# Kernel tuning notes

Measured on AMD Instinct MI355X. Metric: run time of the kernel, lower is better.

The kernel has to match this reference:

```python
import jax, jax.numpy as jnp
import numpy as np

D_MODEL = 1024
NUM_HEADS = 16

def _dense_params(key, d_in, d_out):
    kw, _ = jax.random.split(key)
    # flax default: lecun_normal kernel, zeros bias
    W = jax.random.normal(kw, (d_in, d_out), dtype=jnp.float32) / np.sqrt(d_in)
    b = jnp.zeros((d_out,), dtype=jnp.float32)
    return W, b

def setup_inputs() -> dict:
    key = jax.random.key(0)
    ks = jax.random.split(key, 8)
    B, Tx, Tc = 2, 2048, 2048
    x = jax.random.normal(ks[0], (B, Tx, D_MODEL), dtype=jnp.float32)
    context = jax.random.normal(ks[1], (B, Tc, D_MODEL), dtype=jnp.float32)
    Wq, bq = _dense_params(ks[2], D_MODEL, D_MODEL)
    Wks, bks = _dense_params(ks[3], D_MODEL, D_MODEL)
    Wvs, bvs = _dense_params(ks[4], D_MODEL, D_MODEL)
    Wkc, bkc = _dense_params(ks[5], D_MODEL, D_MODEL)
    Wvc, bvc = _dense_params(ks[6], D_MODEL, D_MODEL)
    Wo, bo = _dense_params(ks[7], D_MODEL, D_MODEL)
    return {"x": x, "context": context,
            "Wq": Wq, "bq": bq, "Wks": Wks, "bks": bks, "Wvs": Wvs, "bvs": bvs,
            "Wkc": Wkc, "bkc": bkc, "Wvc": Wvc, "bvc": bvc, "Wo": Wo, "bo": bo}

def _split_heads(t, H):
    B, T, C = t.shape
    return t.reshape(B, T, H, C // H).transpose(0, 2, 1, 3)  # [B,H,T,hd]

def reference(x, context, Wq, bq, Wks, bks, Wvs, bvs, Wkc, bkc, Wvc, bvc, Wo, bo):
    H = NUM_HEADS
    head_dim = D_MODEL // H
    q = x @ Wq + bq
    k = jnp.concatenate([x @ Wks + bks, context @ Wkc + bkc], axis=1)
    v = jnp.concatenate([x @ Wvs + bvs, context @ Wvc + bvc], axis=1)
    q = _split_heads(q, H)  # [B,H,Tq,hd]
    k = _split_heads(k, H)  # [B,H,Tk,hd]
    v = _split_heads(v, H)
    attn = jnp.einsum('bhqd,bhkd->bhqk', q, k) / jnp.sqrt(jnp.float32(head_dim))
    attn = jax.nn.softmax(attn, axis=-1)
    out = jnp.einsum('bhqk,bhkd->bhqd', attn, v)
    B, _, Tq, _ = out.shape
    out = out.transpose(0, 2, 1, 3).reshape(B, Tq, D_MODEL)
    return out @ Wo + bo
```

## Files before the change

kernel.cpp:

```cpp
#include <hip/hip_runtime.h>
#include <hip/hip_bf16.h>
#include <math.h>


typedef _Float16 f16;
typedef _Float16 f16x8 __attribute__((ext_vector_type(8)));
typedef _Float16 f16x4v __attribute__((ext_vector_type(4)));
typedef float    f32x4 __attribute__((ext_vector_type(4)));

#define MFMA_F16(a, b, c) __builtin_amdgcn_mfma_f32_16x16x32_f16((a), (b), (c), 0, 0, 0)

#define QSCALE 0.18033688011112042f

__device__ __forceinline__ void glds16(const f16* g, f16* l) {
    __builtin_amdgcn_global_load_lds(
        (const __attribute__((address_space(1))) void*)g,
        (__attribute__((address_space(3))) void*)l, 16, 0, 0);
}

__global__ __launch_bounds__(256) void prep(
    const float4* __restrict__ x, const float4* __restrict__ ctx,
    f16x4v* __restrict__ xb, f16x4v* __restrict__ cb,
    const float* __restrict__ W0, const float* __restrict__ W1,
    const float* __restrict__ W2, const float* __restrict__ W3,
    const float* __restrict__ W4, const float* __restrict__ W5,
    f16* __restrict__ wt)
{
    if (blockIdx.x < 8192) {
        const int n4 = (2 * 2048 * 1024) / 4;
        int i = blockIdx.x * 256 + threadIdx.x;
        float4 v;
        f16x4v* dst;
        if (i < n4) { v = x[i];        dst = xb + i; }
        else        { v = ctx[i - n4]; dst = cb + (i - n4); }
        f16x4v h = { (f16)v.x, (f16)v.y, (f16)v.z, (f16)v.w };
        *dst = h;
        return;
    }
    const int idx = blockIdx.x - 8192;
    const int z = idx >> 10, rem = idx & 1023;
    const float* Ws[6] = { W0, W1, W2, W3, W4, W5 };
    const float* W = Ws[z];
    f16* Wt = wt + (size_t)z * (1024 * 1024);

    __shared__ float tile[32][33];
    const int tx = threadIdx.x & 31, ty = threadIdx.x >> 5;
    const int n0 = (rem & 31) * 32, k0 = (rem >> 5) * 32;

#pragma unroll
    for (int i = 0; i < 4; ++i) {
        int r = i * 8 + ty;
        tile[r][tx] = W[(size_t)(k0 + r) * 1024 + n0 + tx];
    }
    __syncthreads();
#pragma unroll
    for (int i = 0; i < 4; ++i) {
        int r = i * 8 + ty;
        Wt[(size_t)(n0 + r) * 1024 + k0 + tx] = (f16)tile[tx][r];
    }
}

#define GEMM_PROLOGUE(BN)                                                     \
    const int m0 = blockIdx.x * 128, n0 = blockIdx.y * (BN);                  \
    const int tid = threadIdx.x;                                              \
    const int w = tid >> 6, lane = tid & 63, quad = lane >> 4, l15 = lane & 15;\
    const int wm = (w >> 1) * 64, wn = (w & 1) * ((BN) / 2);                  \
    const int qsw = (quad ^ ((l15 >> 1) & 3)) * 8;                            \
    int gA[2], gB[(BN) / 64];                                                 \
    _Pragma("unroll")                                                         \
    for (int p = 0; p < 2; ++p) {                                             \
        int s = tid + p * 256;                                                \
        int r = (s >> 2) & 127, c = (s & 3) ^ ((s >> 3) & 3);                 \
        gA[p] = (m0 + r) * 1024 + c * 8;                                      \
    }                                                                         \
    _Pragma("unroll")                                                         \
    for (int p = 0; p < (BN) / 64; ++p) {                                     \
        int s = tid + p * 256;                                                \
        int r = (s >> 2) & ((BN) - 1), c = (s & 3) ^ ((s >> 3) & 3);          \
        gB[p] = (n0 + r) * 1024 + c * 8;                                      \
    }

#define GEMM_STAGE(BN)                                                        \
    __syncthreads();                                                          \
    _Pragma("unroll")                                                         \
    for (int p = 0; p < 2; ++p) glds16(&A[gA[p] + k0], &As[(p * 256 + w * 64) * 8]); \
    _Pragma("unroll")                                                         \
    for (int p = 0; p < (BN) / 64; ++p) glds16(&Bt[gB[p] + k0], &Bs[(p * 256 + w * 64) * 8]); \
    __syncthreads();

__global__ __launch_bounds__(256) void proj_gemm(
    const f16* __restrict__ xb, const f16* __restrict__ cb,
    const f16* __restrict__ wt,
    const float* __restrict__ bq, const float* __restrict__ bks,
    const float* __restrict__ bkc, const float* __restrict__ bvs,
    const float* __restrict__ bvc,
    f16* __restrict__ qbuf, f16* __restrict__ kbuf, f16* __restrict__ vbuf)
{
    __shared__ alignas(16) f16 As[128 * 32];
    __shared__ alignas(16) f16 Bs[128 * 32];

    const int z = blockIdx.z;
    const f16* A = (z == 0 || z == 1 || z == 3) ? xb : cb;
    const int wslot = (z == 0) ? 0 : (z == 1) ? 1 : (z == 2) ? 3 : (z == 3) ? 2 : 4;
    const f16* Bt = wt + (size_t)wslot * 1048576;
    const float* bias = (z == 0) ? bq : (z == 1) ? bks : (z == 2) ? bkc
                        : (z == 3) ? bvs : bvc;
    const int roff = (z == 2 || z == 4) ? 2048 : 0;

    GEMM_PROLOGUE(128)
    f32x4 acc[4][4] = {};

    for (int k0 = 0; k0 < 1024; k0 += 32) {
        GEMM_STAGE(128)
        f16x8 a[4], b[4];
#pragma unroll
        for (int i = 0; i < 4; ++i)
            a[i] = *(const f16x8*)&As[(wm + i * 16 + l15) * 32 + qsw];
#pragma unroll
        for (int i = 0; i < 4; ++i)
            b[i] = *(const f16x8*)&Bs[(wn + i * 16 + l15) * 32 + qsw];
#pragma unroll
        for (int mi = 0; mi < 4; ++mi)
#pragma unroll
            for (int ni = 0; ni < 4; ++ni)
                acc[mi][ni] = MFMA_F16(a[mi], b[ni], acc[mi][ni]);
    }

#pragma unroll
    for (int mi = 0; mi < 4; ++mi) {
#pragma unroll
        for (int r = 0; r < 4; ++r) {
            int row = m0 + wm + mi * 16 + quad * 4 + r;
            int b_ = row >> 11, tok = row & 2047;
#pragma unroll
            for (int ni = 0; ni < 4; ++ni) {
                int col = n0 + wn + ni * 16 + l15;
                float v = acc[mi][ni][r] + bias[col];
                int bh = b_ * 16 + (col >> 6);
                int tg = roff + tok;
                if (z == 0) {
                    qbuf[((size_t)bh * 2048 + tok) * 64 + (col & 63)] = (f16)(v * QSCALE);
                } else if (z <= 2) {
                    kbuf[(size_t)bh * 262144 + (size_t)(tg >> 6) * 4096
                         + (size_t)((col >> 5) & 1) * 2048 + (tg & 63) * 32 + (col & 31)] = (f16)v;
                } else {
                    vbuf[(size_t)bh * 262144 + (size_t)tg * 64 + (col & 63)] = (f16)v;
                }
            }
        }
    }
}

__global__ __launch_bounds__(256) void transpose_v(
    const f16* __restrict__ vbuf, f16* __restrict__ vt)
{
    const int t = threadIdx.x;
    const int mt = t >> 3, md = t & 7;
    const int tok0 = blockIdx.x * 256 + mt * 8;
    const int z = blockIdx.y;
    f16x8 in[8];
#pragma unroll
    for (int i = 0; i < 8; ++i)
        in[i] = *(const f16x8*)&vbuf[((size_t)z * 4096 + tok0 + i) * 64 + md * 8];
    f16x8 ov[8];
#pragma unroll
    for (int j = 0; j < 8; ++j)
#pragma unroll
        for (int i = 0; i < 8; ++i) ov[j][i] = in[i][j];
    const int kt = tok0 >> 6, kks = (tok0 >> 5) & 1, kko = tok0 & 31;
#pragma unroll
    for (int j = 0; j < 8; ++j)
        *(f16x8*)&vt[(size_t)z * 262144 + (size_t)kt * 4096 + kks * 2048
                     + (md * 8 + j) * 32 + kko] = ov[j];
}

__global__ __launch_bounds__(128) void attn_kernel(
    const f16* __restrict__ q, const f16* __restrict__ kb,
    const f16* __restrict__ vtb, f16* __restrict__ o)
{
    __shared__ alignas(16) f16 K_lds[2][4096];
    __shared__ alignas(16) f16 V_lds[2][4096];
    __shared__ alignas(16) f16 P_lds[2][64 * 72];

    const int tid = threadIdx.x;
    const int w = tid >> 6, lane = tid & 63, quad = lane >> 4, l15 = lane & 15;
    const int bh = blockIdx.x, qt = blockIdx.y;
    const int b = bh >> 4, h = bh & 15;
    const int qbase = qt * 128;

    f16x8 qa[4][2];
#pragma unroll
    for (int nq = 0; nq < 4; ++nq) {
        const size_t qaddr =
            ((size_t)bh * 2048 + qbase + w * 64 + nq * 16 + l15) * 64 + quad * 8;
        qa[nq][0] = *(const f16x8*)&q[qaddr];
        qa[nq][1] = *(const f16x8*)&q[qaddr + 32];
    }

    f16x8 ones;
#pragma unroll
    for (int j = 0; j < 8; ++j) ones[j] = (f16)1.0f;

    f32x4 o_acc[4][4] = {};
    f32x4 l_acc[4] = {};

    const f16* ktile = kb + (size_t)bh * 262144;
    const f16* vtile = vtb + (size_t)bh * 262144;

    int goff[4];
#pragma unroll
    for (int p = 0; p < 4; ++p) {
        int c = p * 128 + tid;
        goff[p] = (c >> 2) * 32 + (((c & 3) ^ ((c >> 3) & 3)) * 8);
    }
    const int qsw = (quad ^ ((l15 >> 1) & 3)) * 8;
    f16* Pw = &P_lds[w][0];

#pragma unroll
    for (int p = 0; p < 4; ++p) {
        glds16(ktile + goff[p], &K_lds[0][(p * 128 + w * 64) * 8]);
        glds16(vtile + goff[p], &V_lds[0][(p * 128 + w * 64) * 8]);
    }

    for (int kt = 0; kt < 64; ++kt) {
        const f16* Kc = K_lds[kt & 1];
        const f16* Vc = V_lds[kt & 1];
        f16* Kn = K_lds[(kt + 1) & 1];
        f16* Vn = V_lds[(kt + 1) & 1];

        __syncthreads();

        ktile += 4096; vtile += 4096;
#pragma unroll
        for (int p = 0; p < 4; ++p) {
            glds16(ktile + goff[p], &Kn[(p * 128 + w * 64) * 8]);
            glds16(vtile + goff[p], &Vn[(p * 128 + w * 64) * 8]);
        }

#pragma unroll
        for (int mt = 0; mt < 4; ++mt) {
            f16x8 ka0 = *(const f16x8*)&Kc[(mt * 16 + l15) * 32 + qsw];
            f16x8 ka1 = *(const f16x8*)&Kc[2048 + (mt * 16 + l15) * 32 + qsw];
            f32x4 s[4];
#pragma unroll
            for (int nq = 0; nq < 4; ++nq) {
                f32x4 t = {};
                t = MFMA_F16(ka0, qa[nq][0], t);
                t = MFMA_F16(ka1, qa[nq][1], t);
                s[nq] = t;
            }
#pragma unroll
            for (int nq = 0; nq < 4; ++nq) {
                f16x4v pk;
#pragma unroll
                for (int r = 0; r < 4; ++r)
                    pk[r] = (f16)__builtin_amdgcn_exp2f(s[nq][r]);
                *(f16x4v*)&Pw[(nq * 16 + l15) * 72 + mt * 16 + quad * 4] = pk;
            }
        }

        f16x8 pa[4][2];
#pragma unroll
        for (int nq = 0; nq < 4; ++nq)
#pragma unroll
            for (int ks = 0; ks < 2; ++ks)
                pa[nq][ks] = *(const f16x8*)&Pw[(nq * 16 + l15) * 72 + ks * 32 + quad * 8];

#pragma unroll
        for (int nq = 0; nq < 4; ++nq) {
            l_acc[nq] = MFMA_F16(ones, pa[nq][0], l_acc[nq]);
            l_acc[nq] = MFMA_F16(ones, pa[nq][1], l_acc[nq]);
        }

#pragma unroll
        for (int dt = 0; dt < 4; ++dt) {
            f16x8 vb0 = *(const f16x8*)&Vc[(dt * 16 + l15) * 32 + qsw];
            f16x8 vb1 = *(const f16x8*)&Vc[2048 + (dt * 16 + l15) * 32 + qsw];
#pragma unroll
            for (int nq = 0; nq < 4; ++nq) {
                o_acc[nq][dt] = MFMA_F16(pa[nq][0], vb0, o_acc[nq][dt]);
                o_acc[nq][dt] = MFMA_F16(pa[nq][1], vb1, o_acc[nq][dt]);
            }
        }
    }

#pragma unroll
    for (int nq = 0; nq < 4; ++nq) {
#pragma unroll
        for (int r = 0; r < 4; ++r) {
            float lr = __shfl(l_acc[nq][0], quad * 4 + r, 64);
            float inv = 1.0f / lr;
            int ql = w * 64 + nq * 16 + quad * 4 + r;
            size_t obase = ((size_t)(b * 2048 + qbase + ql)) * 1024 + h * 64;
#pragma unroll
            for (int dt = 0; dt < 4; ++dt)
                o[obase + dt * 16 + l15] = (f16)(o_acc[nq][dt][r] * inv);
        }
    }
}

__global__ __launch_bounds__(256) void out_gemm(
    const f16* __restrict__ abuf, const f16* __restrict__ wt5,
    const float* __restrict__ bo, float* __restrict__ out)
{
    __shared__ alignas(16) f16 As[128 * 32];
    __shared__ alignas(16) f16 Bs[64 * 32];

    const f16* A = abuf;
    const f16* Bt = wt5;

    GEMM_PROLOGUE(64)
    f32x4 acc[4][2] = {};

    for (int k0 = 0; k0 < 1024; k0 += 32) {
        GEMM_STAGE(64)
        f16x8 a[4], b[2];
#pragma unroll
        for (int i = 0; i < 4; ++i)
            a[i] = *(const f16x8*)&As[(wm + i * 16 + l15) * 32 + qsw];
#pragma unroll
        for (int i = 0; i < 2; ++i)
            b[i] = *(const f16x8*)&Bs[(wn + i * 16 + l15) * 32 + qsw];
#pragma unroll
        for (int mi = 0; mi < 4; ++mi)
#pragma unroll
            for (int ni = 0; ni < 2; ++ni)
                acc[mi][ni] = MFMA_F16(a[mi], b[ni], acc[mi][ni]);
    }

#pragma unroll
    for (int mi = 0; mi < 4; ++mi) {
#pragma unroll
        for (int r = 0; r < 4; ++r) {
            int row = m0 + wm + mi * 16 + quad * 4 + r;
#pragma unroll
            for (int ni = 0; ni < 2; ++ni) {
                int col = n0 + wn + ni * 16 + l15;
                out[(size_t)row * 1024 + col] = acc[mi][ni][r] + bo[col];
            }
        }
    }
}

extern "C" void kernel_launch(void* const* d_in, const int* in_sizes, int n_in,
                              void* d_out, int out_size, void* d_ws, size_t ws_size,
                              hipStream_t stream)
{
    (void)in_sizes; (void)n_in; (void)out_size; (void)ws_size;

    const float* x    = (const float*)d_in[0];
    const float* ctx  = (const float*)d_in[1];
    const float* Wq   = (const float*)d_in[2];  const float* bq  = (const float*)d_in[3];
    const float* Wks  = (const float*)d_in[4];  const float* bks = (const float*)d_in[5];
    const float* Wvs  = (const float*)d_in[6];  const float* bvs = (const float*)d_in[7];
    const float* Wkc  = (const float*)d_in[8];  const float* bkc = (const float*)d_in[9];
    const float* Wvc  = (const float*)d_in[10]; const float* bvc = (const float*)d_in[11];
    const float* Wo   = (const float*)d_in[12]; const float* bo  = (const float*)d_in[13];

    char* ws = (char*)d_ws;
    f16* xb   = (f16*)(ws + 0);
    f16* cb   = (f16*)(ws + 8388608);
    f16* vt   = (f16*)(ws + 0);
    f16* wt   = (f16*)(ws + 16777216);
    f16* qbuf = (f16*)(ws + 29360128);
    f16* kbuf = (f16*)(ws + 37748736);
    f16* vbuf = (f16*)(ws + 54525952);
    f16* abuf = (f16*)(ws + 71303168);

    prep<<<14336, 256, 0, stream>>>((const float4*)x, (const float4*)ctx,
                                    (f16x4v*)xb, (f16x4v*)cb,
                                    Wq, Wks, Wvs, Wkc, Wvc, Wo, wt);

    proj_gemm<<<dim3(32, 8, 5), 256, 0, stream>>>(
        xb, cb, wt, bq, bks, bkc, bvs, bvc, qbuf, kbuf, vbuf);

    transpose_v<<<dim3(16, 32), 256, 0, stream>>>(vbuf, vt);

    attn_kernel<<<dim3(32, 16), 128, 0, stream>>>(qbuf, kbuf, vt, abuf);

    out_gemm<<<dim3(32, 16), 256, 0, stream>>>(abuf, wt + 5 * 1048576, bo, (float*)d_out);
}
```

Baseline: 362.6 us.

## Split attention over two KV halves with 4-wave blocks and a combine kernel

The attention kernel now splits the key/value sequence into two halves across a new grid dimension. Each block runs four waves of 32 queries instead of two waves of 64, so there are more blocks and waves in flight. Each split writes a normalized partial output and its row sums into reused workspace regions. A new combine kernel then merges the two partials, weighted by their row sums, into the head-interleaved layout. This trades an extra kernel launch and a round trip of the partial outputs through memory for higher occupancy and parallelism on the main attention loop.

```diff
diff --git a/kernel.cpp b/kernel.cpp
--- a/kernel.cpp
+++ b/kernel.cpp
@@ -174,25 +174,25 @@
                      + (md * 8 + j) * 32 + kko] = ov[j];
 }
 
-__global__ __launch_bounds__(128) void attn_kernel(
+__global__ __launch_bounds__(256, 2) void attn_kernel(
     const f16* __restrict__ q, const f16* __restrict__ kb,
-    const f16* __restrict__ vtb, f16* __restrict__ o)
+    const f16* __restrict__ vtb, f16* __restrict__ osplit,
+    float* __restrict__ lsplit)
 {
     __shared__ alignas(16) f16 K_lds[2][4096];
     __shared__ alignas(16) f16 V_lds[2][4096];
-    __shared__ alignas(16) f16 P_lds[2][64 * 72];
+    __shared__ alignas(16) f16 P_lds[128 * 72];
 
     const int tid = threadIdx.x;
     const int w = tid >> 6, lane = tid & 63, quad = lane >> 4, l15 = lane & 15;
-    const int bh = blockIdx.x, qt = blockIdx.y;
-    const int b = bh >> 4, h = bh & 15;
+    const int bh = blockIdx.x, qt = blockIdx.y, sp = blockIdx.z;
     const int qbase = qt * 128;
 
-    f16x8 qa[4][2];
-#pragma unroll
-    for (int nq = 0; nq < 4; ++nq) {
+    f16x8 qa[2][2];
+#pragma unroll
+    for (int nq = 0; nq < 2; ++nq) {
         const size_t qaddr =
-            ((size_t)bh * 2048 + qbase + w * 64 + nq * 16 + l15) * 64 + quad * 8;
+            ((size_t)bh * 2048 + qbase + w * 32 + nq * 16 + l15) * 64 + quad * 8;
         qa[nq][0] = *(const f16x8*)&q[qaddr];
         qa[nq][1] = *(const f16x8*)&q[qaddr + 32];
     }
@@ -201,28 +201,22 @@
 #pragma unroll
     for (int j = 0; j < 8; ++j) ones[j] = (f16)1.0f;
 
-    f32x4 o_acc[4][4] = {};
-    f32x4 l_acc[4] = {};
-
-    const f16* ktile = kb + (size_t)bh * 262144;
-    const f16* vtile = vtb + (size_t)bh * 262144;
-
-    int goff[4];
-#pragma unroll
-    for (int p = 0; p < 4; ++p) {
-        int c = p * 128 + tid;
-        goff[p] = (c >> 2) * 32 + (((c & 3) ^ ((c >> 3) & 3)) * 8);
-    }
+    f32x4 o_acc[2][4] = {};
+    f32x4 l_acc[2] = {};
+
+    const f16* ktile = kb + (size_t)bh * 262144 + (size_t)sp * 131072;
+    const f16* vtile = vtb + (size_t)bh * 262144 + (size_t)sp * 131072;
+
+    const int sco = ((tid >> 2) * 4 + ((tid & 3) ^ ((tid >> 3) & 3))) * 8;
     const int qsw = (quad ^ ((l15 >> 1) & 3)) * 8;
-    f16* Pw = &P_lds[w][0];
-
-#pragma unroll
-    for (int p = 0; p < 4; ++p) {
-        glds16(ktile + goff[p], &K_lds[0][(p * 128 + w * 64) * 8]);
-        glds16(vtile + goff[p], &V_lds[0][(p * 128 + w * 64) * 8]);
-    }
-
-    for (int kt = 0; kt < 64; ++kt) {
+    const int wslot = w * 512;
+
+    glds16(ktile + sco,        &K_lds[0][wslot]);
+    glds16(ktile + 2048 + sco, &K_lds[0][2048 + wslot]);
+    glds16(vtile + sco,        &V_lds[0][wslot]);
+    glds16(vtile + 2048 + sco, &V_lds[0][2048 + wslot]);
+
+    for (int kt = 0; kt < 32; ++kt) {
         const f16* Kc = K_lds[kt & 1];
         const f16* Vc = V_lds[kt & 1];
         f16* Kn = K_lds[(kt + 1) & 1];
@@ -231,43 +225,46 @@
         __syncthreads();
 
         ktile += 4096; vtile += 4096;
-#pragma unroll
-        for (int p = 0; p < 4; ++p) {
-            glds16(ktile + goff[p], &Kn[(p * 128 + w * 64) * 8]);
-            glds16(vtile + goff[p], &Vn[(p * 128 + w * 64) * 8]);
-        }
-
+        glds16(ktile + sco,        Kn + wslot);
+        glds16(ktile + 2048 + sco, Kn + 2048 + wslot);
+        glds16(vtile + sco,        Vn + wslot);
+        glds16(vtile + 2048 + sco, Vn + 2048 + wslot);
+
+        f32x4 s[4][2];
 #pragma unroll
         for (int mt = 0; mt < 4; ++mt) {
             f16x8 ka0 = *(const f16x8*)&Kc[(mt * 16 + l15) * 32 + qsw];
             f16x8 ka1 = *(const f16x8*)&Kc[2048 + (mt * 16 + l15) * 32 + qsw];
-            f32x4 s[4];
-#pragma unroll
-            for (int nq = 0; nq < 4; ++nq) {
+#pragma unroll
+            for (int nq = 0; nq < 2; ++nq) {
                 f32x4 t = {};
                 t = MFMA_F16(ka0, qa[nq][0], t);
                 t = MFMA_F16(ka1, qa[nq][1], t);
-                s[nq] = t;
+                s[mt][nq] = t;
             }
-#pragma unroll
-            for (int nq = 0; nq < 4; ++nq) {
+        }
+
+#pragma unroll
+        for (int mt = 0; mt < 4; ++mt) {
+#pragma unroll
+            for (int nq = 0; nq < 2; ++nq) {
                 f16x4v pk;
 #pragma unroll
                 for (int r = 0; r < 4; ++r)
-                    pk[r] = (f16)__builtin_amdgcn_exp2f(s[nq][r]);
-                *(f16x4v*)&Pw[(nq * 16 + l15) * 72 + mt * 16 + quad * 4] = pk;
+                    pk[r] = (f16)__builtin_amdgcn_exp2f(s[mt][nq][r]);
+                *(f16x4v*)&P_lds[(w * 32 + nq * 16 + l15) * 72 + mt * 16 + quad * 4] = pk;
             }
         }
 
-        f16x8 pa[4][2];
-#pragma unroll
-        for (int nq = 0; nq < 4; ++nq)
+        f16x8 pa[2][2];
+#pragma unroll
+        for (int nq = 0; nq < 2; ++nq)
 #pragma unroll
             for (int ks = 0; ks < 2; ++ks)
-                pa[nq][ks] = *(const f16x8*)&Pw[(nq * 16 + l15) * 72 + ks * 32 + quad * 8];
-
-#pragma unroll
-        for (int nq = 0; nq < 4; ++nq) {
+                pa[nq][ks] = *(const f16x8*)&P_lds[(w * 32 + nq * 16 + l15) * 72 + ks * 32 + quad * 8];
+
+#pragma unroll
+        for (int nq = 0; nq < 2; ++nq) {
             l_acc[nq] = MFMA_F16(ones, pa[nq][0], l_acc[nq]);
             l_acc[nq] = MFMA_F16(ones, pa[nq][1], l_acc[nq]);
         }
@@ -277,26 +274,53 @@
             f16x8 vb0 = *(const f16x8*)&Vc[(dt * 16 + l15) * 32 + qsw];
             f16x8 vb1 = *(const f16x8*)&Vc[2048 + (dt * 16 + l15) * 32 + qsw];
 #pragma unroll
-            for (int nq = 0; nq < 4; ++nq) {
+            for (int nq = 0; nq < 2; ++nq) {
                 o_acc[nq][dt] = MFMA_F16(pa[nq][0], vb0, o_acc[nq][dt]);
                 o_acc[nq][dt] = MFMA_F16(pa[nq][1], vb1, o_acc[nq][dt]);
             }
         }
     }
 
-#pragma unroll
-    for (int nq = 0; nq < 4; ++nq) {
+    const size_t sb = (size_t)(sp * 32 + bh) * 2048 + qbase;
+#pragma unroll
+    for (int nq = 0; nq < 2; ++nq) {
+        if (quad == 0)
+            lsplit[sb + w * 32 + nq * 16 + l15] = l_acc[nq][0];
 #pragma unroll
         for (int r = 0; r < 4; ++r) {
             float lr = __shfl(l_acc[nq][0], quad * 4 + r, 64);
             float inv = 1.0f / lr;
-            int ql = w * 64 + nq * 16 + quad * 4 + r;
-            size_t obase = ((size_t)(b * 2048 + qbase + ql)) * 1024 + h * 64;
+            int ql = w * 32 + nq * 16 + quad * 4 + r;
+            size_t obase = (sb + ql) * 64;
 #pragma unroll
             for (int dt = 0; dt < 4; ++dt)
-                o[obase + dt * 16 + l15] = (f16)(o_acc[nq][dt][r] * inv);
-        }
-    }
+                osplit[obase + dt * 16 + l15] = (f16)(o_acc[nq][dt][r] * inv);
+        }
+    }
+}
+
+__global__ __launch_bounds__(256) void combine(
+    const f16* __restrict__ osplit, const float* __restrict__ lsplit,
+    f16* __restrict__ abuf)
+{
+    int idx = blockIdx.x * 256 + threadIdx.x;
+    int d8 = idx & 7;
+    int row = (idx >> 3) & 2047;
+    int bh = idx >> 14;
+    int b = bh >> 4, h = bh & 15;
+    size_t base1 = ((size_t)bh * 2048 + row) * 64 + d8 * 8;
+    size_t base2 = ((size_t)(32 + bh) * 2048 + row) * 64 + d8 * 8;
+    float l1 = lsplit[bh * 2048 + row];
+    float l2 = lsplit[(32 + bh) * 2048 + row];
+    float inv = 1.0f / (l1 + l2);
+    float w1 = l1 * inv, w2 = l2 * inv;
+    f16x8 a = *(const f16x8*)&osplit[base1];
+    f16x8 c = *(const f16x8*)&osplit[base2];
+    f16x8 out;
+#pragma unroll
+    for (int j = 0; j < 8; ++j)
+        out[j] = (f16)(w1 * (float)a[j] + w2 * (float)c[j]);
+    *(f16x8*)&abuf[((size_t)(b * 2048 + row)) * 1024 + h * 64 + d8 * 8] = out;
 }
 
 __global__ __launch_bounds__(256) void out_gemm(
@@ -358,14 +382,16 @@
     const float* Wo   = (const float*)d_in[12]; const float* bo  = (const float*)d_in[13];
 
     char* ws = (char*)d_ws;
-    f16* xb   = (f16*)(ws + 0);
-    f16* cb   = (f16*)(ws + 8388608);
-    f16* vt   = (f16*)(ws + 0);
-    f16* wt   = (f16*)(ws + 16777216);
-    f16* qbuf = (f16*)(ws + 29360128);
-    f16* kbuf = (f16*)(ws + 37748736);
-    f16* vbuf = (f16*)(ws + 54525952);
-    f16* abuf = (f16*)(ws + 71303168);
+    f16*   xb     = (f16*)(ws + 0);
+    f16*   cb     = (f16*)(ws + 8388608);
+    f16*   vt     = (f16*)(ws + 0);
+    f16*   wt     = (f16*)(ws + 16777216);
+    float* lsplit = (float*)(ws + 16777216);
+    f16*   qbuf   = (f16*)(ws + 29360128);
+    f16*   kbuf   = (f16*)(ws + 37748736);
+    f16*   vbuf   = (f16*)(ws + 54525952);
+    f16*   osplit = (f16*)(ws + 54525952);
+    f16*   abuf   = (f16*)(ws + 71303168);
 
     prep<<<14336, 256, 0, stream>>>((const float4*)x, (const float4*)ctx,
                                     (f16x4v*)xb, (f16x4v*)cb,
@@ -376,7 +402,9 @@
 
     transpose_v<<<dim3(16, 32), 256, 0, stream>>>(vbuf, vt);
 
-    attn_kernel<<<dim3(32, 16), 128, 0, stream>>>(qbuf, kbuf, vt, abuf);
+    attn_kernel<<<dim3(32, 16, 2), 256, 0, stream>>>(qbuf, kbuf, vt, osplit, lsplit);
+
+    combine<<<2048, 256, 0, stream>>>(osplit, lsplit, abuf);
 
     out_gemm<<<dim3(32, 16), 256, 0, stream>>>(abuf, wt + 5 * 1048576, bo, (float*)d_out);
 }
```

Result: faster. 317.5 us (-12.4%).
